# Optimization experiments

Measured on AMD Instinct MI355X. Metric: run time of the kernel, lower is better.

Reference implementation:

```python
import jax, jax.numpy as jnp
import numpy as np

WH, WW = 12, 12
N_TOK = WH * WW          # 144
DIM = 512
HEADS = 16
NW = 64                  # windows per image
B_ = 256                 # num_windows * batch
CPB_HIDDEN = 512


def _rel_tables():
    # continuous relative coords table (SwinV2 cpb input), shape (1, 2Wh-1, 2Ww-1, 2)
    ch = np.arange(-(WH - 1), WH, dtype=np.float32)
    cw = np.arange(-(WW - 1), WW, dtype=np.float32)
    gh, gw = np.meshgrid(ch, cw, indexing='ij')
    table = np.stack([gh, gw], axis=-1)[None]
    table[..., 0] /= (WH - 1)
    table[..., 1] /= (WW - 1)
    table *= 8.0
    table = np.sign(table) * np.log2(np.abs(table) + 1.0) / np.log2(8.0)
    # relative position index, shape (N, N), values in [0, (2Wh-1)*(2Ww-1))
    coords = np.stack(np.meshgrid(np.arange(WH), np.arange(WW), indexing='ij'))
    cf = coords.reshape(2, -1)
    rel = (cf[:, :, None] - cf[:, None, :]).transpose(1, 2, 0).astype(np.int64)
    rel[..., 0] += WH - 1
    rel[..., 1] += WW - 1
    rel[..., 0] *= 2 * WW - 1
    idx = rel.sum(-1)
    return table.astype(np.float32), idx


def setup_inputs() -> dict:
    key = jax.random.key(0)
    ks = jax.random.split(key, 10)
    table, idx = _rel_tables()
    x = jax.random.normal(ks[0], (B_, N_TOK, DIM), dtype=jnp.float32)
    # 0 / -100 additive mask (shifted-window style), shape (nW, N, N)
    mask = jnp.where(jax.random.uniform(ks[1], (NW, N_TOK, N_TOK)) < 0.9, 0.0, -100.0).astype(jnp.float32)
    s = 0.02
    return {
        'x': x,
        'mask': mask,
        'qkv_w': s * jax.random.normal(ks[2], (3 * DIM, DIM), dtype=jnp.float32),
        'qkv_b': jnp.zeros((3 * DIM,), dtype=jnp.float32),
        'proj_w': s * jax.random.normal(ks[3], (DIM, DIM), dtype=jnp.float32),
        'proj_b': jnp.zeros((DIM,), dtype=jnp.float32),
        'cpb_w1': s * jax.random.normal(ks[4], (CPB_HIDDEN, 2), dtype=jnp.float32),
        'cpb_b1': jnp.zeros((CPB_HIDDEN,), dtype=jnp.float32),
        'cpb_w2': s * jax.random.normal(ks[5], (HEADS, CPB_HIDDEN), dtype=jnp.float32),
        'rel_table': jnp.asarray(table),
        'rel_index': jnp.asarray(idx, dtype=jnp.int32),
    }


def reference(x, mask, qkv_w, qkv_b, proj_w, proj_b, cpb_w1, cpb_b1, cpb_w2, rel_table, rel_index):
    Bw, N, C = x.shape
    H = cpb_w2.shape[0]
    hd = C // H
    scale = hd ** -0.5
    qkv = (x @ qkv_w.T + qkv_b).reshape(Bw, N, 3, H, hd).transpose(2, 0, 3, 1, 4)
    q, k, v = qkv[0], qkv[1], qkv[2]          # each (Bw, H, N, hd)
    attn = jnp.einsum('bhnd,bhmd->bhnm', q * scale, k)
    # continuous relative position bias: MLP on coord table then gather
    tbl = jax.nn.relu(rel_table @ cpb_w1.T + cpb_b1) @ cpb_w2.T   # (1, 2Wh-1, 2Ww-1, H)
    tbl = tbl.reshape(-1, H)
    bias = tbl[rel_index.reshape(-1)].reshape(N, N, H).transpose(2, 0, 1)  # (H, N, N)
    attn = attn + bias[None]
    nW = mask.shape[0]
    attn = attn.reshape(Bw // nW, nW, H, N, N) + mask[None, :, None]
    attn = jax.nn.softmax(attn.reshape(Bw, H, N, N), axis=-1)
    out = jnp.einsum('bhnm,bhmd->bhnd', attn, v).transpose(0, 2, 1, 3).reshape(Bw, N, C)
    return out @ proj_w.T + proj_b
```

## Files before the change

### kernel.cpp

```cpp
#include <hip/hip_runtime.h>


using f32x4  = __attribute__((ext_vector_type(4))) float;
using bf16x8 = __attribute__((ext_vector_type(8))) short;

__device__ __forceinline__ unsigned short f2bf(float f) {
  unsigned u = __float_as_uint(f);
  u = (u + 0x7fffu + ((u >> 16) & 1u)) >> 16;
  return (unsigned short)u;
}
__device__ __forceinline__ float bf2f(unsigned short s) {
  return __uint_as_float(((unsigned)s) << 16);
}

typedef __attribute__((address_space(1))) unsigned int as1_u32;
typedef __attribute__((address_space(3))) unsigned int as3_u32;

__device__ __forceinline__ void gll16(const void* g, void* l) {
  __builtin_amdgcn_global_load_lds((const as1_u32*)g, (as3_u32*)l, 16, 0, 0);
}

__global__ void cvt_f32_bf16(const float4* __restrict__ in,
                             unsigned short* __restrict__ out, int n4) {
  int i = blockIdx.x * blockDim.x + threadIdx.x;
  int stride = gridDim.x * blockDim.x;
  for (; i < n4; i += stride) {
    float4 v = in[i];
    ushort4 o;
    o.x = f2bf(v.x); o.y = f2bf(v.y); o.z = f2bf(v.z); o.w = f2bf(v.w);
    *(ushort4*)(out + (size_t)i * 4) = o;
  }
}

__global__ void cpb_mlp(const float* __restrict__ tbl_in,
                        const float* __restrict__ w1,
                        const float* __restrict__ b1,
                        const float* __restrict__ w2,
                        float* __restrict__ tbl_out) {
  __shared__ float hid[512];
  const int p = blockIdx.x;
  const int t = threadIdx.x;
  float t0 = tbl_in[p * 2 + 0], t1 = tbl_in[p * 2 + 1];
  float hv = fmaf(w1[t * 2 + 0], t0, fmaf(w1[t * 2 + 1], t1, b1[t]));
  hid[t] = fmaxf(hv, 0.f);
  __syncthreads();
  const int head = t >> 5, j = t & 31;
  float partial = 0.f;
  for (int i = j; i < 512; i += 32) partial += hid[i] * w2[head * 512 + i];
#pragma unroll
  for (int mk = 16; mk >= 1; mk >>= 1) partial += __shfl_xor(partial, mk, 32);
  if (j == 0) tbl_out[p * 16 + head] = partial;
}

__global__ void bias_gather(const float* __restrict__ tbl,
                            const int* __restrict__ idx,
                            unsigned short* __restrict__ bias_bf) {
  int f = blockIdx.x * 256 + threadIdx.x;
  if (f >= 16 * 20736) return;
  int h = f / 20736;
  int p = f - h * 20736;
  bias_bf[f] = f2bf(tbl[idx[p] * 16 + h]);
}

template <bool OUT_BF16, bool QSCALE>
__global__ __launch_bounds__(256) void gemm_bt_k(
    const unsigned short* __restrict__ A, const unsigned short* __restrict__ B,
    const float* __restrict__ bias, void* __restrict__ C, int N, int K) {
  __shared__ __align__(16) unsigned short As[128 * 32];
  __shared__ __align__(16) unsigned short Bs[128 * 32];
  const int tid = threadIdx.x;
  const int wave = tid >> 6, lane = tid & 63;
  const int m0 = blockIdx.y << 7, n0 = blockIdx.x << 7;
  const int wr = wave >> 1, wc = wave & 1;
  const int l15 = lane & 15, l4 = lane >> 4;

  f32x4 acc[4][4] = {};

  const unsigned short* gA = A + (size_t)(m0 + wave * 32 + (lane >> 2)) * K + (lane & 3) * 8;
  const unsigned short* gB = B + (size_t)(n0 + wave * 32 + (lane >> 2)) * K + (lane & 3) * 8;
  unsigned short* lA = As + wave * 32 * 32;
  unsigned short* lB = Bs + wave * 32 * 32;

  for (int k0 = 0; k0 < K; k0 += 32) {
    __syncthreads();
    gll16(gA + k0, lA);
    gll16(gA + k0 + (size_t)16 * K, lA + 16 * 32);
    gll16(gB + k0, lB);
    gll16(gB + k0 + (size_t)16 * K, lB + 16 * 32);
    __syncthreads();
    bf16x8 af[4], bfr[4];
#pragma unroll
    for (int t = 0; t < 4; ++t) {
      af[t]  = *(const bf16x8*)(As + (wr * 64 + t * 16 + l15) * 32 + l4 * 8);
      bfr[t] = *(const bf16x8*)(Bs + (wc * 64 + t * 16 + l15) * 32 + l4 * 8);
    }
#pragma unroll
    for (int i = 0; i < 4; ++i)
#pragma unroll
      for (int j = 0; j < 4; ++j)
        acc[i][j] = __builtin_amdgcn_mfma_f32_16x16x32_bf16(af[i], bfr[j], acc[i][j], 0, 0, 0);
  }

#pragma unroll
  for (int i = 0; i < 4; ++i) {
    int rowb = m0 + wr * 64 + i * 16 + l4 * 4;
#pragma unroll
    for (int j = 0; j < 4; ++j) {
      int col = n0 + wc * 64 + j * 16 + l15;
      float bv = bias[col];
#pragma unroll
      for (int r = 0; r < 4; ++r) {
        size_t off = (size_t)(rowb + r) * N + col;
        float v = acc[i][j][r] + bv;
        if (QSCALE && col < 512) v *= 0.17677669529663688f;
        if (OUT_BF16) ((unsigned short*)C)[off] = f2bf(v);
        else          ((float*)C)[off] = v;
      }
    }
  }
}

__global__ __launch_bounds__(256) void attn_k(
    const unsigned short* __restrict__ qkv,
    const unsigned short* __restrict__ maskbf,
    const unsigned short* __restrict__ biasbf,
    unsigned short* __restrict__ aout) {
  __shared__ __align__(16) unsigned short P[144 * 152];
  __shared__ __align__(16) unsigned short Vt[32 * 152];

  const int h = blockIdx.x, b = blockIdx.y;
  const int tid = threadIdx.x;
  const int wave = tid >> 6, lane = tid & 63;
  const int l15 = lane & 15, l4 = lane >> 4;
  const size_t base = (size_t)b * 144 * 1536;

  for (int c = tid; c < 576; c += 256) {
    int dblk = c / 144;
    int m = c - dblk * 144;
    uint4 v = *(const uint4*)(qkv + base + (size_t)m * 1536 + 1024 + h * 32 + dblk * 8);
    unsigned short tmp[8];
    *(uint4*)tmp = v;
#pragma unroll
    for (int j = 0; j < 8; ++j) Vt[(dblk * 8 + j) * 152 + m] = tmp[j];
  }

  const unsigned short* mrow = maskbf + (size_t)(b & 63) * 20736;
  const unsigned short* brow = biasbf + (size_t)h * 20736;
  for (int rt = wave; rt < 9; rt += 4) {
    const int n = rt * 16 + l15;
    bf16x8 qf = *(const bf16x8*)(qkv + base + (size_t)n * 1536 + h * 32 + l4 * 8);
    f32x4 acc[9];
#pragma unroll
    for (int kt = 0; kt < 9; ++kt) {
      bf16x8 kf = *(const bf16x8*)(qkv + base + (size_t)(kt * 16 + l15) * 1536 + 512 + h * 32 + l4 * 8);
      const int mq = kt * 16 + l4 * 4;
      ushort4 mv = *(const ushort4*)(mrow + n * 144 + mq);
      ushort4 bv = *(const ushort4*)(brow + n * 144 + mq);
      f32x4 ci;
      ci[0] = bf2f(mv.x) + bf2f(bv.x);
      ci[1] = bf2f(mv.y) + bf2f(bv.y);
      ci[2] = bf2f(mv.z) + bf2f(bv.z);
      ci[3] = bf2f(mv.w) + bf2f(bv.w);
      acc[kt] = __builtin_amdgcn_mfma_f32_16x16x32_bf16(kf, qf, ci, 0, 0, 0);
    }
    float mx = -3.0e38f;
#pragma unroll
    for (int kt = 0; kt < 9; ++kt)
#pragma unroll
      for (int r = 0; r < 4; ++r) mx = fmaxf(mx, acc[kt][r]);
    mx = fmaxf(mx, __shfl_xor(mx, 16));
    mx = fmaxf(mx, __shfl_xor(mx, 32));
    float sum = 0.f;
#pragma unroll
    for (int kt = 0; kt < 9; ++kt)
#pragma unroll
      for (int r = 0; r < 4; ++r) {
        float p = __expf(acc[kt][r] - mx);
        acc[kt][r] = p;
        sum += p;
      }
    sum += __shfl_xor(sum, 16);
    sum += __shfl_xor(sum, 32);
    float inv = 1.0f / sum;
    unsigned short* prow = P + n * 152;
#pragma unroll
    for (int kt = 0; kt < 9; ++kt) {
      ushort4 o;
      o.x = f2bf(acc[kt][0] * inv);
      o.y = f2bf(acc[kt][1] * inv);
      o.z = f2bf(acc[kt][2] * inv);
      o.w = f2bf(acc[kt][3] * inv);
      *(ushort4*)(prow + kt * 16 + l4 * 4) = o;
    }
  }
  __syncthreads();

  for (int tt = wave; tt < 18; tt += 4) {
    int rt = tt >> 1, dj = tt & 1;
    f32x4 c = {0.f, 0.f, 0.f, 0.f};
    const unsigned short* pa = P + (rt * 16 + l15) * 152;
    const unsigned short* vb = Vt + (dj * 16 + l15) * 152;
#pragma unroll
    for (int ks = 0; ks < 4; ++ks) {
      bf16x8 ap = *(const bf16x8*)(pa + ks * 32 + l4 * 8);
      bf16x8 bv = *(const bf16x8*)(vb + ks * 32 + l4 * 8);
      c = __builtin_amdgcn_mfma_f32_16x16x32_bf16(ap, bv, c, 0, 0, 0);
    }
    {
      bf16x8 ap = {}, bv = {};
      if (l4 < 2) {
        ap = *(const bf16x8*)(pa + 128 + l4 * 8);
        bv = *(const bf16x8*)(vb + 128 + l4 * 8);
      }
      c = __builtin_amdgcn_mfma_f32_16x16x32_bf16(ap, bv, c, 0, 0, 0);
    }
#pragma unroll
    for (int r = 0; r < 4; ++r) {
      int n = rt * 16 + l4 * 4 + r;
      int d = dj * 16 + l15;
      aout[((size_t)(b * 144 + n)) * 512 + h * 32 + d] = f2bf(c[r]);
    }
  }
}

extern "C" void kernel_launch(void* const* d_in, const int* in_sizes, int n_in,
                              void* d_out, int out_size, void* d_ws, size_t ws_size,
                              hipStream_t stream) {
  const float* x        = (const float*)d_in[0];
  const float* mask     = (const float*)d_in[1];
  const float* qkv_w    = (const float*)d_in[2];
  const float* qkv_b    = (const float*)d_in[3];
  const float* proj_w   = (const float*)d_in[4];
  const float* proj_b   = (const float*)d_in[5];
  const float* cpb_w1   = (const float*)d_in[6];
  const float* cpb_b1   = (const float*)d_in[7];
  const float* cpb_w2   = (const float*)d_in[8];
  const float* rel_tab  = (const float*)d_in[9];
  const int*   rel_idx  = (const int*)d_in[10];
  float* out = (float*)d_out;

  char* ws = (char*)d_ws;
  unsigned short* x_bf    = (unsigned short*)(ws);
  unsigned short* wq_bf   = (unsigned short*)(ws + 37748736);
  unsigned short* wp_bf   = (unsigned short*)(ws + 39321600);
  unsigned short* qkv_ws  = (unsigned short*)(ws + 39845888);
  unsigned short* attn_ws = (unsigned short*)(ws + 153092096);
  float*          tbl_ws  = (float*)(ws + 190840832);
  unsigned short* maskbf  = (unsigned short*)(ws + 190874688);
  unsigned short* biasbf  = (unsigned short*)(ws + 193528896);

  cvt_f32_bf16<<<2048, 256, 0, stream>>>((const float4*)x, x_bf, 4718592);
  cvt_f32_bf16<<<768, 256, 0, stream>>>((const float4*)qkv_w, wq_bf, 196608);
  cvt_f32_bf16<<<256, 256, 0, stream>>>((const float4*)proj_w, wp_bf, 65536);
  cvt_f32_bf16<<<1296, 256, 0, stream>>>((const float4*)mask, maskbf, 331776);

  cpb_mlp<<<529, 512, 0, stream>>>(rel_tab, cpb_w1, cpb_b1, cpb_w2, tbl_ws);
  bias_gather<<<1296, 256, 0, stream>>>(tbl_ws, rel_idx, biasbf);

  gemm_bt_k<true, true><<<dim3(12, 288), 256, 0, stream>>>(
      x_bf, wq_bf, qkv_b, (void*)qkv_ws, 1536, 512);

  attn_k<<<dim3(16, 256), 256, 0, stream>>>(qkv_ws, maskbf, biasbf, attn_ws);

  gemm_bt_k<false, false><<<dim3(4, 288), 256, 0, stream>>>(
      attn_ws, wp_bf, proj_b, (void*)out, 512, 512);
}
```

Measured before the change: 407.6 us.

## Streamline attention softmax with exp2, deferred normalization and LDS-staged K

Folds log2(e) into the Q scale, mask and bias so softmax can use exp2. Drops the row-max subtraction and moves the 1/sum scaling into the PV output stage, using packed bf16 conversion. K tiles are staged into swizzled LDS with global_load_lds, and blocks are remapped so heads of the same window run close together for cache reuse. The separate mask conversion kernel is removed by reading the fp32 mask directly. The risk is overflow without max subtraction if logits grow large, plus extra fp32 traffic for mask and bias.

```diff
diff --git a/kernel.cpp b/kernel.cpp
--- a/kernel.cpp
+++ b/kernel.cpp
@@ -3,14 +3,30 @@
 
 using f32x4  = __attribute__((ext_vector_type(4))) float;
 using bf16x8 = __attribute__((ext_vector_type(8))) short;
+
+#define LOG2E 1.4426950408889634f
+
+#if __has_builtin(__builtin_amdgcn_exp2f)
+#define EXP2(x) __builtin_amdgcn_exp2f(x)
+#else
+#define EXP2(x) __expf((x) * 0.6931471805599453f)
+#endif
+#if __has_builtin(__builtin_amdgcn_rcpf)
+#define RCP(x) __builtin_amdgcn_rcpf(x)
+#else
+#define RCP(x) (1.0f / (x))
+#endif
 
 __device__ __forceinline__ unsigned short f2bf(float f) {
   unsigned u = __float_as_uint(f);
   u = (u + 0x7fffu + ((u >> 16) & 1u)) >> 16;
   return (unsigned short)u;
 }
-__device__ __forceinline__ float bf2f(unsigned short s) {
-  return __uint_as_float(((unsigned)s) << 16);
+
+__device__ __forceinline__ unsigned cvt_pk_bf16(float lo, float hi) {
+  unsigned r;
+  asm("v_cvt_pk_bf16_f32 %0, %1, %2" : "=v"(r) : "v"(lo), "v"(hi));
+  return r;
 }
 
 typedef __attribute__((address_space(1))) unsigned int as1_u32;
@@ -54,12 +70,12 @@
 
 __global__ void bias_gather(const float* __restrict__ tbl,
                             const int* __restrict__ idx,
-                            unsigned short* __restrict__ bias_bf) {
+                            float* __restrict__ bias_f) {
   int f = blockIdx.x * 256 + threadIdx.x;
   if (f >= 16 * 20736) return;
   int h = f / 20736;
   int p = f - h * 20736;
-  bias_bf[f] = f2bf(tbl[idx[p] * 16 + h]);
+  bias_f[f] = tbl[idx[p] * 16 + h] * LOG2E;
 }
 
 template <bool OUT_BF16, bool QSCALE>
@@ -112,7 +128,7 @@
       for (int r = 0; r < 4; ++r) {
         size_t off = (size_t)(rowb + r) * N + col;
         float v = acc[i][j][r] + bv;
-        if (QSCALE && col < 512) v *= 0.17677669529663688f;
+        if (QSCALE && col < 512) v *= 0.17677669529663688f * LOG2E;
         if (OUT_BF16) ((unsigned short*)C)[off] = f2bf(v);
         else          ((float*)C)[off] = v;
       }
@@ -120,19 +136,78 @@
   }
 }
 
-__global__ __launch_bounds__(256) void attn_k(
+__global__ __launch_bounds__(256, 3) void attn_k(
     const unsigned short* __restrict__ qkv,
-    const unsigned short* __restrict__ maskbf,
-    const unsigned short* __restrict__ biasbf,
+    const float* __restrict__ maskf,
+    const float* __restrict__ biasf,
     unsigned short* __restrict__ aout) {
-  __shared__ __align__(16) unsigned short P[144 * 152];
-  __shared__ __align__(16) unsigned short Vt[32 * 152];
-
-  const int h = blockIdx.x, b = blockIdx.y;
+  __shared__ __align__(16) char smem[53568];
+  unsigned short* Ks  = (unsigned short*)smem;
+  unsigned short* Vt  = (unsigned short*)smem;
+  float*          invs = (float*)(smem + 9216);
+  unsigned short* P   = (unsigned short*)(smem + 9792);
+
+  const int lid = blockIdx.x;
+  const int xc = lid & 7, slot = lid >> 3;
+  const int b = (xc << 5) + (slot >> 4);
+  const int h = slot & 15;
+
   const int tid = threadIdx.x;
   const int wave = tid >> 6, lane = tid & 63;
   const int l15 = lane & 15, l4 = lane >> 4;
   const size_t base = (size_t)b * 144 * 1536;
+
+  for (int c = wave; c < 9; c += 4) {
+    int s = c * 64 + lane;
+    int r = s >> 2;
+    int halfd = (s & 3) ^ ((r >> 1) & 3);
+    gll16(qkv + base + (size_t)r * 1536 + 512 + h * 32 + halfd * 8,
+          Ks + c * 512);
+  }
+  __syncthreads();
+
+  const float* mrow = maskf + (size_t)(b & 63) * 20736;
+  const float* brow = biasf + (size_t)h * 20736;
+  for (int rt = wave; rt < 9; rt += 4) {
+    const int n = rt * 16 + l15;
+    bf16x8 qf = *(const bf16x8*)(qkv + base + (size_t)n * 1536 + h * 32 + l4 * 8);
+    f32x4 acc[9];
+#pragma unroll
+    for (int kt = 0; kt < 9; ++kt) {
+      const int mq = kt * 16 + l4 * 4;
+      float4 mv = *(const float4*)(mrow + n * 144 + mq);
+      float4 bv = *(const float4*)(brow + n * 144 + mq);
+      f32x4 ci;
+      ci[0] = fmaf(mv.x, LOG2E, bv.x);
+      ci[1] = fmaf(mv.y, LOG2E, bv.y);
+      ci[2] = fmaf(mv.z, LOG2E, bv.z);
+      ci[3] = fmaf(mv.w, LOG2E, bv.w);
+      int r = kt * 16 + l15;
+      bf16x8 kf = *(const bf16x8*)(Ks + (((r << 2) + (l4 ^ ((r >> 1) & 3))) << 3));
+      acc[kt] = __builtin_amdgcn_mfma_f32_16x16x32_bf16(kf, qf, ci, 0, 0, 0);
+    }
+    float sum = 0.f;
+#pragma unroll
+    for (int kt = 0; kt < 9; ++kt)
+#pragma unroll
+      for (int r = 0; r < 4; ++r) {
+        float p = EXP2(acc[kt][r]);
+        acc[kt][r] = p;
+        sum += p;
+      }
+    sum += __shfl_xor(sum, 16);
+    sum += __shfl_xor(sum, 32);
+    if (l4 == 0) invs[n] = RCP(sum);
+    unsigned short* prow = P + n * 152;
+#pragma unroll
+    for (int kt = 0; kt < 9; ++kt) {
+      uint2 w;
+      w.x = cvt_pk_bf16(acc[kt][0], acc[kt][1]);
+      w.y = cvt_pk_bf16(acc[kt][2], acc[kt][3]);
+      *(uint2*)(prow + kt * 16 + l4 * 4) = w;
+    }
+  }
+  __syncthreads();
 
   for (int c = tid; c < 576; c += 256) {
     int dblk = c / 144;
@@ -141,57 +216,7 @@
     unsigned short tmp[8];
     *(uint4*)tmp = v;
 #pragma unroll
-    for (int j = 0; j < 8; ++j) Vt[(dblk * 8 + j) * 152 + m] = tmp[j];
-  }
-
-  const unsigned short* mrow = maskbf + (size_t)(b & 63) * 20736;
-  const unsigned short* brow = biasbf + (size_t)h * 20736;
-  for (int rt = wave; rt < 9; rt += 4) {
-    const int n = rt * 16 + l15;
-    bf16x8 qf = *(const bf16x8*)(qkv + base + (size_t)n * 1536 + h * 32 + l4 * 8);
-    f32x4 acc[9];
-#pragma unroll
-    for (int kt = 0; kt < 9; ++kt) {
-      bf16x8 kf = *(const bf16x8*)(qkv + base + (size_t)(kt * 16 + l15) * 1536 + 512 + h * 32 + l4 * 8);
-      const int mq = kt * 16 + l4 * 4;
-      ushort4 mv = *(const ushort4*)(mrow + n * 144 + mq);
-      ushort4 bv = *(const ushort4*)(brow + n * 144 + mq);
-      f32x4 ci;
-      ci[0] = bf2f(mv.x) + bf2f(bv.x);
-      ci[1] = bf2f(mv.y) + bf2f(bv.y);
-      ci[2] = bf2f(mv.z) + bf2f(bv.z);
-      ci[3] = bf2f(mv.w) + bf2f(bv.w);
-      acc[kt] = __builtin_amdgcn_mfma_f32_16x16x32_bf16(kf, qf, ci, 0, 0, 0);
-    }
-    float mx = -3.0e38f;
-#pragma unroll
-    for (int kt = 0; kt < 9; ++kt)
-#pragma unroll
-      for (int r = 0; r < 4; ++r) mx = fmaxf(mx, acc[kt][r]);
-    mx = fmaxf(mx, __shfl_xor(mx, 16));
-    mx = fmaxf(mx, __shfl_xor(mx, 32));
-    float sum = 0.f;
-#pragma unroll
-    for (int kt = 0; kt < 9; ++kt)
-#pragma unroll
-      for (int r = 0; r < 4; ++r) {
-        float p = __expf(acc[kt][r] - mx);
-        acc[kt][r] = p;
-        sum += p;
-      }
-    sum += __shfl_xor(sum, 16);
-    sum += __shfl_xor(sum, 32);
-    float inv = 1.0f / sum;
-    unsigned short* prow = P + n * 152;
-#pragma unroll
-    for (int kt = 0; kt < 9; ++kt) {
-      ushort4 o;
-      o.x = f2bf(acc[kt][0] * inv);
-      o.y = f2bf(acc[kt][1] * inv);
-      o.z = f2bf(acc[kt][2] * inv);
-      o.w = f2bf(acc[kt][3] * inv);
-      *(ushort4*)(prow + kt * 16 + l4 * 4) = o;
-    }
+    for (int j = 0; j < 8; ++j) Vt[(dblk * 8 + j) * 144 + m] = tmp[j];
   }
   __syncthreads();
 
@@ -199,7 +224,7 @@
     int rt = tt >> 1, dj = tt & 1;
     f32x4 c = {0.f, 0.f, 0.f, 0.f};
     const unsigned short* pa = P + (rt * 16 + l15) * 152;
-    const unsigned short* vb = Vt + (dj * 16 + l15) * 152;
+    const unsigned short* vb = Vt + (dj * 16 + l15) * 144;
 #pragma unroll
     for (int ks = 0; ks < 4; ++ks) {
       bf16x8 ap = *(const bf16x8*)(pa + ks * 32 + l4 * 8);
@@ -218,7 +243,8 @@
     for (int r = 0; r < 4; ++r) {
       int n = rt * 16 + l4 * 4 + r;
       int d = dj * 16 + l15;
-      aout[((size_t)(b * 144 + n)) * 512 + h * 32 + d] = f2bf(c[r]);
+      float iv = invs[n];
+      aout[((size_t)(b * 144 + n)) * 512 + h * 32 + d] = f2bf(c[r] * iv);
     }
   }
 }
@@ -246,21 +272,19 @@
   unsigned short* qkv_ws  = (unsigned short*)(ws + 39845888);
   unsigned short* attn_ws = (unsigned short*)(ws + 153092096);
   float*          tbl_ws  = (float*)(ws + 190840832);
-  unsigned short* maskbf  = (unsigned short*)(ws + 190874688);
-  unsigned short* biasbf  = (unsigned short*)(ws + 193528896);
+  float*          biasf   = (float*)(ws + 190874688);
 
   cvt_f32_bf16<<<2048, 256, 0, stream>>>((const float4*)x, x_bf, 4718592);
   cvt_f32_bf16<<<768, 256, 0, stream>>>((const float4*)qkv_w, wq_bf, 196608);
   cvt_f32_bf16<<<256, 256, 0, stream>>>((const float4*)proj_w, wp_bf, 65536);
-  cvt_f32_bf16<<<1296, 256, 0, stream>>>((const float4*)mask, maskbf, 331776);
 
   cpb_mlp<<<529, 512, 0, stream>>>(rel_tab, cpb_w1, cpb_b1, cpb_w2, tbl_ws);
-  bias_gather<<<1296, 256, 0, stream>>>(tbl_ws, rel_idx, biasbf);
+  bias_gather<<<1296, 256, 0, stream>>>(tbl_ws, rel_idx, biasf);
 
   gemm_bt_k<true, true><<<dim3(12, 288), 256, 0, stream>>>(
       x_bf, wq_bf, qkv_b, (void*)qkv_ws, 1536, 512);
 
-  attn_k<<<dim3(16, 256), 256, 0, stream>>>(qkv_ws, maskbf, biasbf, attn_ws);
+  attn_k<<<4096, 256, 0, stream>>>(qkv_ws, mask, biasf, attn_ws);
 
   gemm_bt_k<false, false><<<dim3(4, 288), 256, 0, stream>>>(
       attn_ws, wp_bf, proj_b, (void*)out, 512, 512);
```

Result: faster. 374.4 us (-8.2%).
